# Kernel optimization log

Hardware: AMD Instinct MI355X
Metric: run time of the kernel (lower is better)

Reference implementation:

```python
import jax, jax.numpy as jnp
import numpy as np

EPS = 1e-6


def _rms_norm(x, w):
    # RMSNorm over last dim in fp32, like Qwen3RMSNorm
    x32 = x.astype(jnp.float32)
    var = jnp.mean(x32 * x32, axis=-1, keepdims=True)
    return (x32 * jax.lax.rsqrt(var + EPS)).astype(x.dtype) * w


def _rotate_half(x):
    h = x.shape[-1] // 2
    return jnp.concatenate([-x[..., h:], x[..., :h]], axis=-1)


def setup_inputs() -> dict:
    key = jax.random.key(0)
    ks = jax.random.split(key, 8)
    B, S, HID = 1, 8192, 1024
    H, HKV, D = 16, 8, 128
    n_seg = 8
    hidden_states = jax.random.normal(ks[0], (B, S, HID), dtype=jnp.float32)
    cu_seqlens = jnp.arange(n_seg + 1, dtype=jnp.int32) * (S // n_seg)
    # multimodal RoPE tables: two position streams, each [B, S, D]
    inv_freq = 1.0 / (1e6 ** (jnp.arange(0, D, 2, dtype=jnp.float32) / D))
    pos = jnp.arange(S, dtype=jnp.float32)
    ang0 = pos[:, None] * inv_freq[None, :]            # [S, D/2]
    ang1 = (pos[:, None] * 0.5) * inv_freq[None, :]    # second stream
    def tab(a):
        return jnp.concatenate([a, a], axis=-1)[None]   # [1, S, D]
    cos = jnp.stack([tab(jnp.cos(ang0)), tab(jnp.cos(ang1))], axis=0)  # [2,1,S,D]
    sin = jnp.stack([tab(jnp.sin(ang0)), tab(jnp.sin(ang1))], axis=0)
    sd = 0.02
    Wq = jax.random.normal(ks[1], (H * D, HID), dtype=jnp.float32) * sd
    Wk = jax.random.normal(ks[2], (HKV * D, HID), dtype=jnp.float32) * sd
    Wv = jax.random.normal(ks[3], (HKV * D, HID), dtype=jnp.float32) * sd
    Wo = jax.random.normal(ks[4], (HID, H * D), dtype=jnp.float32) * sd
    q_norm_w = 1.0 + jax.random.normal(ks[5], (D,), dtype=jnp.float32) * sd
    k_norm_w = 1.0 + jax.random.normal(ks[6], (D,), dtype=jnp.float32) * sd
    return {"hidden_states": hidden_states, "cu_seqlens": cu_seqlens,
            "cos": cos, "sin": sin, "Wq": Wq, "Wk": Wk, "Wv": Wv, "Wo": Wo,
            "q_norm_w": q_norm_w, "k_norm_w": k_norm_w}


def reference(hidden_states, cu_seqlens, cos, sin, Wq, Wk, Wv, Wo, q_norm_w, k_norm_w):
    B, S, _ = hidden_states.shape
    D = q_norm_w.shape[0]
    H = Wq.shape[0] // D
    HKV = Wk.shape[0] // D
    groups = H // HKV
    n_seg = cu_seqlens.shape[0] - 1   # equal-length segments (static)
    L = S // n_seg
    scaling = D ** -0.5

    # projections -> [B, H(kv), S, D]
    q = (hidden_states @ Wq.T).reshape(B, S, H, D).transpose(0, 2, 1, 3)
    k = (hidden_states @ Wk.T).reshape(B, S, HKV, D).transpose(0, 2, 1, 3)
    v = (hidden_states @ Wv.T).reshape(B, S, HKV, D).transpose(0, 2, 1, 3)

    q = _rms_norm(q, q_norm_w)
    k = _rms_norm(k, k_norm_w)

    # multimodal RoPE: interleave the two streams across the two half-dims
    half = D // 2
    cos_e = jnp.concatenate([cos[0, ..., :half], cos[1, ..., half:]], axis=-1)[:, None]  # [B,1,S,D]
    sin_e = jnp.concatenate([sin[0, ..., :half], sin[1, ..., half:]], axis=-1)[:, None]
    q = q * cos_e + _rotate_half(q) * sin_e
    k = k * cos_e + _rotate_half(k) * sin_e

    # GQA: repeat kv heads
    k = jnp.repeat(k, groups, axis=1)
    v = jnp.repeat(v, groups, axis=1)

    # block-diagonal attention over cu_seqlens segments (equal-length -> reshape)
    qb = q.reshape(B, H, n_seg, L, D)
    kb = k.reshape(B, H, n_seg, L, D)
    vb = v.reshape(B, H, n_seg, L, D)
    scores = jnp.einsum('bhnld,bhnmd->bhnlm', qb, kb) * scaling
    probs = jax.nn.softmax(scores, axis=-1)
    ob = jnp.einsum('bhnlm,bhnmd->bhnld', probs, vb)
    out = ob.reshape(B, H, S, D).transpose(0, 2, 1, 3).reshape(B, S, H * D)
    return out @ Wo.T
```

## Files before the change

kernel.cpp:

```cpp
#include <hip/hip_runtime.h>

#define S_LEN 8192
#define HID   1024
#define NH    16
#define NKV   8
#define HD    128
#define LSEG  1024

typedef float  f4  __attribute__((ext_vector_type(4)));
typedef _Float16 h4 __attribute__((ext_vector_type(4)));
typedef _Float16 h8 __attribute__((ext_vector_type(8)));

__device__ __forceinline__ void gl_lds16(const void* g, void* l) {
  __builtin_amdgcn_global_load_lds((const __attribute__((address_space(1))) void*)g,
                                   (__attribute__((address_space(3))) void*)l, 16, 0, 0);
}

__device__ __forceinline__ h8 ld8u(const _Float16* p) {
  h4 a = *(const h4*)p;
  h4 b = *(const h4*)(p + 4);
  return __builtin_shufflevector(a, b, 0, 1, 2, 3, 4, 5, 6, 7);
}

template <int CTRL>
__device__ __forceinline__ float dppf(float v) {
  return __builtin_bit_cast(float,
      __builtin_amdgcn_mov_dpp(__builtin_bit_cast(int, v), CTRL, 0xF, 0xF, true));
}
__device__ __forceinline__ float red16_max(float x) {
  x = fmaxf(x, dppf<0xB1>(x));
  x = fmaxf(x, dppf<0x4E>(x));
  x = fmaxf(x, dppf<0x141>(x));
  x = fmaxf(x, dppf<0x140>(x));
  return x;
}
__device__ __forceinline__ float red16_sum(float x) {
  x += dppf<0xB1>(x);
  x += dppf<0x4E>(x);
  x += dppf<0x141>(x);
  x += dppf<0x140>(x);
  return x;
}
__device__ __forceinline__ float bcast16(float v) {
  return __builtin_bit_cast(float,
      __builtin_amdgcn_ds_swizzle(__builtin_bit_cast(int, v), 0x0010));
}

__global__ void convert_kernel(const float* __restrict__ hid, const float* __restrict__ wq,
                               const float* __restrict__ wk, const float* __restrict__ wv,
                               const float* __restrict__ wo,
                               _Float16* __restrict__ hid16, _Float16* __restrict__ wqkv,
                               _Float16* __restrict__ wo16) {
  const int total4 = 3670016;
  for (int i = blockIdx.x * blockDim.x + threadIdx.x; i < total4; i += gridDim.x * blockDim.x) {
    int i4 = i * 4;
    const float* src; _Float16* dst;
    if      (i4 <  8388608) { src = hid + i4;              dst = hid16 + i4; }
    else if (i4 < 10485760) { src = wq + (i4 -  8388608);  dst = wqkv + (i4 - 8388608); }
    else if (i4 < 11534336) { src = wk + (i4 - 10485760);  dst = wqkv + 2097152 + (i4 - 10485760); }
    else if (i4 < 12582912) { src = wv + (i4 - 11534336);  dst = wqkv + 3145728 + (i4 - 11534336); }
    else                    { src = wo + (i4 - 12582912);  dst = wo16 + (i4 - 12582912); }
    f4 x = *(const f4*)src;
    h4 y; y[0]=(_Float16)x[0]; y[1]=(_Float16)x[1]; y[2]=(_Float16)x[2]; y[3]=(_Float16)x[3];
    *(h4*)dst = y;
  }
}

template <int FUSED>
__global__ __launch_bounds__(256, 3)
void gemm_kernel(const _Float16* __restrict__ A, const _Float16* __restrict__ B,
                 float* __restrict__ Cout, int K, int N,
                 const float* __restrict__ cosp, const float* __restrict__ sinp,
                 const float* __restrict__ qnw, const float* __restrict__ knw,
                 _Float16* __restrict__ q16, _Float16* __restrict__ k16,
                 _Float16* __restrict__ v16T) {
  __shared__ __align__(16) char smem[32768];

  constexpr int GX  = FUSED ? 32 : 8;
  constexpr int NWG = FUSED ? 2048 : 512;
  const int lin = blockIdx.y * GX + blockIdx.x;
  const int swz = (lin & 7) * (NWG >> 3) + (lin >> 3);
  const int bx = swz & (GX - 1), by = swz / GX;

  const int tid = threadIdx.x, w = tid >> 6, ln = tid & 63;
  const int l15 = ln & 15, l4 = ln >> 4;
  const int m0 = by * 128, n0 = bx * 128;
  const int sg_row = ln >> 2, sg_cho = (ln & 3) * 8;

  f4 acc[2][8] = {};

  for (int k0 = 0; k0 < K; k0 += 64) {
    __syncthreads();
#pragma unroll
    for (int r = 0; r < 2; r++) {
      int ch = r * 4 + w;
#pragma unroll
      for (int u = 0; u < 2; u++) {
        gl_lds16(A + (size_t)(m0 + ch * 16 + sg_row) * K + k0 + u * 32 + sg_cho,
                 smem + u * 8192 + ch * 1024);
        gl_lds16(B + (size_t)(n0 + ch * 16 + sg_row) * K + k0 + u * 32 + sg_cho,
                 smem + 16384 + u * 8192 + ch * 1024);
      }
    }
    __syncthreads();
#pragma unroll
    for (int u = 0; u < 2; u++) {
      const _Float16* As = (const _Float16*)(smem + u * 8192);
      const _Float16* Bs = (const _Float16*)(smem + 16384 + u * 8192);
      h8 af[2], bf[8];
#pragma unroll
      for (int mt = 0; mt < 2; mt++) af[mt] = *(const h8*)(As + (w * 32 + mt * 16 + l15) * 32 + l4 * 8);
#pragma unroll
      for (int nt = 0; nt < 8; nt++) bf[nt] = *(const h8*)(Bs + (nt * 16 + l15) * 32 + l4 * 8);
#pragma unroll
      for (int mt = 0; mt < 2; mt++)
#pragma unroll
        for (int nt = 0; nt < 8; nt++)
          acc[mt][nt] = __builtin_amdgcn_mfma_f32_16x16x32_f16(af[mt], bf[nt], acc[mt][nt], 0, 0, 0);
    }
  }

  if (!FUSED) {
#pragma unroll
    for (int mt = 0; mt < 2; mt++)
#pragma unroll
      for (int rg = 0; rg < 4; rg++) {
        int row = m0 + w * 32 + mt * 16 + l4 * 4 + rg;
#pragma unroll
        for (int nt = 0; nt < 8; nt++)
          Cout[(size_t)row * N + n0 + nt * 16 + l15] = acc[mt][nt][rg];
      }
    return;
  } else {
    const int head = bx;
    if (head < 24) {
      const float* nw = (head < 16) ? qnw : knw;
      const float hs = (head < 16) ? 0.12751734f : 1.0f;
      _Float16* base = (head < 16) ? q16 + (size_t)head * S_LEN * HD
                                   : k16 + (size_t)(head - 16) * S_LEN * HD;
      float nwv[8];
#pragma unroll
      for (int nt = 0; nt < 8; nt++) nwv[nt] = nw[nt * 16 + l15];
#pragma unroll
      for (int mt = 0; mt < 2; mt++)
#pragma unroll
        for (int rg = 0; rg < 4; rg++) {
          const int row = m0 + w * 32 + mt * 16 + l4 * 4 + rg;
          float ss = 0.f;
#pragma unroll
          for (int nt = 0; nt < 8; nt++) ss += acc[mt][nt][rg] * acc[mt][nt][rg];
          ss = red16_sum(ss);
          const float sc = rsqrtf(ss * 0.0078125f + 1e-6f);
#pragma unroll
          for (int nt = 0; nt < 8; nt++) {
            const int c = nt * 16 + l15;
            const int str = (nt >= 4) ? 1048576 : 0;
            float x  = acc[mt][nt][rg] * sc * nwv[nt];
            float xp = acc[mt][nt ^ 4][rg] * sc * nwv[nt ^ 4];
            float ce = cosp[str + row * HD + c];
            float se = sinp[str + row * HD + c];
            float rot = (nt >= 4) ? xp : -xp;
            base[(size_t)row * HD + c] = (_Float16)((x * ce + rot * se) * hs);
          }
        }
    } else {
      _Float16* vb = v16T + (size_t)(head - 24) * S_LEN * HD;
#pragma unroll
      for (int mt = 0; mt < 2; mt++)
#pragma unroll
        for (int nt = 0; nt < 8; nt++) {
          h4 hv;
#pragma unroll
          for (int rg = 0; rg < 4; rg++) hv[rg] = (_Float16)acc[mt][nt][rg];
          *(h4*)&vb[(size_t)(nt * 16 + l15) * S_LEN + m0 + w * 32 + mt * 16 + l4 * 4] = hv;
        }
    }
  }
}

__global__ __launch_bounds__(256, 2)
void attn_kernel(const _Float16* __restrict__ q16, const _Float16* __restrict__ k16,
                 const _Float16* __restrict__ vT, _Float16* __restrict__ ao16) {
  const int bid = blockIdx.x;
  const int xcd = bid & 7, slot = bid >> 3;
  const int grp = xcd * 8 + (slot >> 4);
  const int mem = slot & 15;
  const int g = grp >> 3, hkv = grp & 7;
  const int tq = mem & 7, h = hkv * 2 + (mem >> 3);

  const int tid = threadIdx.x, w = tid >> 6, ln = tid & 63;
  const int l15 = ln & 15, l4 = ln >> 4;

  __shared__ _Float16 Kb[2][64 * 132];
  __shared__ _Float16 Vb[2][128 * 68];

  const _Float16* qsrc = q16 + ((size_t)h * S_LEN + g * LSEG + tq * 128 + w * 32) * HD;
  h8 qf[2][4];
#pragma unroll
  for (int mt = 0; mt < 2; mt++)
#pragma unroll
    for (int kk = 0; kk < 4; kk++)
      qf[mt][kk] = *(const h8*)(qsrc + (size_t)(mt * 16 + l15) * HD + kk * 32 + l4 * 8);

  h8 onesB;
  {
    _Float16 ov = (l15 == 0) ? (_Float16)1.0f : (_Float16)0.0f;
#pragma unroll
    for (int jj = 0; jj < 8; jj++) onesB[jj] = ov;
  }

  f4 O[2][9] = {};
  float mr[2][4];
#pragma unroll
  for (int mt = 0; mt < 2; mt++)
#pragma unroll
    for (int rg = 0; rg < 4; rg++) mr[mt][rg] = -1e30f;

  const size_t kbase = ((size_t)hkv * S_LEN + g * LSEG) * HD;
  const size_t vbase = (size_t)hkv * S_LEN * HD + (size_t)g * LSEG;

  const int krow = tid >> 4, ko = tid & 15;
  const int vd   = tid >> 3, vo = tid & 7;
  const int vrow = w * 32 + (ln >> 1), vcol = (ln & 1) * 32;

  uint4 kr[4], vr[4];
#pragma unroll
  for (int i = 0; i < 4; i++) {
    kr[i] = *(const uint4*)(k16 + kbase + (size_t)(krow + 16 * i) * HD + ko * 8);
    vr[i] = *(const uint4*)(vT + vbase + (size_t)(vd + 32 * i) * S_LEN + vo * 8);
  }
#pragma unroll
  for (int i = 0; i < 4; i++) {
    int row = krow + 16 * i;
    *(uint2*)&Kb[0][row * 132 + ko * 8]     = make_uint2(kr[i].x, kr[i].y);
    *(uint2*)&Kb[0][row * 132 + ko * 8 + 4] = make_uint2(kr[i].z, kr[i].w);
    int d = vd + 32 * i;
    *(uint2*)&Vb[0][d * 68 + vo * 8]     = make_uint2(vr[i].x, vr[i].y);
    *(uint2*)&Vb[0][d * 68 + vo * 8 + 4] = make_uint2(vr[i].z, vr[i].w);
  }

  for (int j = 0; j < 16; j++) {
    __syncthreads();
    const int cur = j & 1, nxt = cur ^ 1;
    const _Float16* Kc = Kb[cur];
    const _Float16* Vc = Vb[cur];
    _Float16* Pb = Vb[nxt];
    _Float16* Kn = Kb[nxt];

    if (j < 15) {
      const int jn = j + 1;
#pragma unroll
      for (int i = 0; i < 4; i++)
        kr[i] = *(const uint4*)(k16 + kbase + (size_t)(jn * 64 + krow + 16 * i) * HD + ko * 8);
#pragma unroll
      for (int c = 0; c < 4; c++)
        vr[c] = *(const uint4*)(vT + vbase + (size_t)vrow * S_LEN + jn * 64 + vcol + c * 8);
    }

    f4 s[2][4] = {};
    __builtin_amdgcn_s_setprio(1);
#pragma unroll
    for (int kk = 0; kk < 4; kk++) {
#pragma unroll
      for (int nt = 0; nt < 4; nt++) {
        h8 b = ld8u(Kc + (nt * 16 + l15) * 132 + kk * 32 + l4 * 8);
        s[0][nt] = __builtin_amdgcn_mfma_f32_16x16x32_f16(qf[0][kk], b, s[0][nt], 0, 0, 0);
        s[1][nt] = __builtin_amdgcn_mfma_f32_16x16x32_f16(qf[1][kk], b, s[1][nt], 0, 0, 0);
      }
    }
    __builtin_amdgcn_s_setprio(0);

    bool nd = false;
#pragma unroll
    for (int mt = 0; mt < 2; mt++)
#pragma unroll
      for (int rg = 0; rg < 4; rg++) {
        float thr = mr[mt][rg] + 8.f;
        nd = nd || (s[mt][0][rg] > thr) || (s[mt][1][rg] > thr) ||
                   (s[mt][2][rg] > thr) || (s[mt][3][rg] > thr);
      }
    const bool needr = __any((int)nd) != 0;
    float al[2][4];
    if (needr) {
#pragma unroll
      for (int mt = 0; mt < 2; mt++)
#pragma unroll
        for (int rg = 0; rg < 4; rg++) {
          float m = fmaxf(fmaxf(s[mt][0][rg], s[mt][1][rg]), fmaxf(s[mt][2][rg], s[mt][3][rg]));
          m = red16_max(m);
          float mnew = fmaxf(mr[mt][rg], m);
          al[mt][rg] = exp2f(mr[mt][rg] - mnew);
          mr[mt][rg] = mnew;
        }
    }
#pragma unroll
    for (int mt = 0; mt < 2; mt++)
#pragma unroll
      for (int rg = 0; rg < 4; rg++)
#pragma unroll
        for (int nt = 0; nt < 4; nt++)
          s[mt][nt][rg] = exp2f(s[mt][nt][rg] - mr[mt][rg]);

#pragma unroll
    for (int mt = 0; mt < 2; mt++)
#pragma unroll
      for (int nt = 0; nt < 4; nt++)
#pragma unroll
        for (int rg = 0; rg < 4; rg++)
          Pb[(w * 32 + mt * 16 + l4 * 4 + rg) * 68 + nt * 16 + l15] = (_Float16)s[mt][nt][rg];
    if (needr) {
#pragma unroll
      for (int mt = 0; mt < 2; mt++)
#pragma unroll
        for (int d8 = 0; d8 < 9; d8++)
#pragma unroll
          for (int rg = 0; rg < 4; rg++) O[mt][d8][rg] *= al[mt][rg];
    }

    __builtin_amdgcn_s_setprio(1);
#pragma unroll
    for (int kk = 0; kk < 2; kk++) {
      h8 a0 = ld8u(Pb + (w * 32 + l15) * 68 + kk * 32 + l4 * 8);
      h8 a1 = ld8u(Pb + (w * 32 + 16 + l15) * 68 + kk * 32 + l4 * 8);
#pragma unroll
      for (int d8 = 0; d8 < 8; d8++) {
        h8 b = ld8u(Vc + (d8 * 16 + l15) * 68 + kk * 32 + l4 * 8);
        O[0][d8] = __builtin_amdgcn_mfma_f32_16x16x32_f16(a0, b, O[0][d8], 0, 0, 0);
        O[1][d8] = __builtin_amdgcn_mfma_f32_16x16x32_f16(a1, b, O[1][d8], 0, 0, 0);
      }
      O[0][8] = __builtin_amdgcn_mfma_f32_16x16x32_f16(a0, onesB, O[0][8], 0, 0, 0);
      O[1][8] = __builtin_amdgcn_mfma_f32_16x16x32_f16(a1, onesB, O[1][8], 0, 0, 0);
    }
    __builtin_amdgcn_s_setprio(0);

    if (j < 15) {
#pragma unroll
      for (int i = 0; i < 4; i++) {
        int row = krow + 16 * i;
        *(uint2*)&Kn[row * 132 + ko * 8]     = make_uint2(kr[i].x, kr[i].y);
        *(uint2*)&Kn[row * 132 + ko * 8 + 4] = make_uint2(kr[i].z, kr[i].w);
      }
#pragma unroll
      for (int c = 0; c < 4; c++) {
        *(uint2*)&Pb[vrow * 68 + vcol + c * 8]     = make_uint2(vr[c].x, vr[c].y);
        *(uint2*)&Pb[vrow * 68 + vcol + c * 8 + 4] = make_uint2(vr[c].z, vr[c].w);
      }
    }
  }

  const size_t obase = (size_t)(g * LSEG + tq * 128);
#pragma unroll
  for (int mt = 0; mt < 2; mt++)
#pragma unroll
    for (int rg = 0; rg < 4; rg++) {
      float inv = 1.f / bcast16(O[mt][8][rg]);
#pragma unroll
      for (int d8 = 0; d8 < 8; d8++)
        ao16[(obase + w * 32 + mt * 16 + l4 * 4 + rg) * 2048 + h * HD + d8 * 16 + l15] =
            (_Float16)(O[mt][d8][rg] * inv);
    }
}

extern "C" void kernel_launch(void* const* d_in, const int* in_sizes, int n_in,
                              void* d_out, int out_size, void* d_ws, size_t ws_size,
                              hipStream_t stream) {
  const float* hid  = (const float*)d_in[0];
  const float* cosp = (const float*)d_in[2];
  const float* sinp = (const float*)d_in[3];
  const float* wq   = (const float*)d_in[4];
  const float* wk   = (const float*)d_in[5];
  const float* wv   = (const float*)d_in[6];
  const float* wo   = (const float*)d_in[7];
  const float* qnw  = (const float*)d_in[8];
  const float* knw  = (const float*)d_in[9];
  float* out = (float*)d_out;

  _Float16* hid16 = (_Float16*)d_ws;
  _Float16* wqkv  = hid16 + 8388608;
  _Float16* wo16  = wqkv + 4194304;
  _Float16* q16   = wo16 + 2097152;
  _Float16* k16   = q16 + 16777216;
  _Float16* v16T  = k16 + 8388608;
  _Float16* ao16  = v16T + 8388608;

  convert_kernel<<<dim3(1024), dim3(256), 0, stream>>>(hid, wq, wk, wv, wo, hid16, wqkv, wo16);
  gemm_kernel<1><<<dim3(32, 64), dim3(256), 0, stream>>>(hid16, wqkv, nullptr, 1024, 4096,
                                                         cosp, sinp, qnw, knw, q16, k16, v16T);
  attn_kernel<<<dim3(1024), dim3(256), 0, stream>>>(q16, k16, v16T, ao16);
  gemm_kernel<0><<<dim3(8, 64), dim3(256), 0, stream>>>(ao16, wo16, out, 2048, 1024,
                                                        nullptr, nullptr, nullptr, nullptr,
                                                        nullptr, nullptr, nullptr);
}
```

Baseline: 366.2 us.

## Double-buffer GEMM K loop and pre-interleave cos/sin RoPE table

The GEMM main loop now processes 32-wide K steps with two LDS buffers, prefetching the next tile via global_load_lds while computing the current one, and uses one barrier per step instead of two. The convert kernel also builds a combined float2 cos/sin table with the mRoPE stream selection already applied, so the fused QKV epilogue does one 8-byte load instead of two scattered loads. The table reuses the attention-output workspace buffer, which attention overwrites afterward. This relies on the trailing barrier of each step to make the prefetched tile visible and adds a small extra pass in the convert kernel.

Result: slower. 386.2 us (+5.4%).

```diff
diff --git a/kernel.cpp b/kernel.cpp
--- a/kernel.cpp
+++ b/kernel.cpp
@@ -49,8 +49,9 @@
 __global__ void convert_kernel(const float* __restrict__ hid, const float* __restrict__ wq,
                                const float* __restrict__ wk, const float* __restrict__ wv,
                                const float* __restrict__ wo,
+                               const float* __restrict__ cosp, const float* __restrict__ sinp,
                                _Float16* __restrict__ hid16, _Float16* __restrict__ wqkv,
-                               _Float16* __restrict__ wo16) {
+                               _Float16* __restrict__ wo16, float2* __restrict__ cs32) {
   const int total4 = 3670016;
   for (int i = blockIdx.x * blockDim.x + threadIdx.x; i < total4; i += gridDim.x * blockDim.x) {
     int i4 = i * 4;
@@ -64,13 +65,17 @@
     h4 y; y[0]=(_Float16)x[0]; y[1]=(_Float16)x[1]; y[2]=(_Float16)x[2]; y[3]=(_Float16)x[3];
     *(h4*)dst = y;
   }
+  for (int i = blockIdx.x * blockDim.x + threadIdx.x; i < 1048576; i += gridDim.x * blockDim.x) {
+    int str = ((i & 127) >= 64) ? 1048576 : 0;
+    cs32[i] = make_float2(cosp[str + i], sinp[str + i]);
+  }
 }
 
 template <int FUSED>
 __global__ __launch_bounds__(256, 3)
 void gemm_kernel(const _Float16* __restrict__ A, const _Float16* __restrict__ B,
                  float* __restrict__ Cout, int K, int N,
-                 const float* __restrict__ cosp, const float* __restrict__ sinp,
+                 const float2* __restrict__ csp,
                  const float* __restrict__ qnw, const float* __restrict__ knw,
                  _Float16* __restrict__ q16, _Float16* __restrict__ k16,
                  _Float16* __restrict__ v16T) {
@@ -89,35 +94,36 @@
 
   f4 acc[2][8] = {};
 
-  for (int k0 = 0; k0 < K; k0 += 64) {
-    __syncthreads();
+  auto stage = [&](int u, int k) {
 #pragma unroll
     for (int r = 0; r < 2; r++) {
       int ch = r * 4 + w;
-#pragma unroll
-      for (int u = 0; u < 2; u++) {
-        gl_lds16(A + (size_t)(m0 + ch * 16 + sg_row) * K + k0 + u * 32 + sg_cho,
-                 smem + u * 8192 + ch * 1024);
-        gl_lds16(B + (size_t)(n0 + ch * 16 + sg_row) * K + k0 + u * 32 + sg_cho,
-                 smem + 16384 + u * 8192 + ch * 1024);
-      }
-    }
+      gl_lds16(A + (size_t)(m0 + ch * 16 + sg_row) * K + k + sg_cho,
+               smem + u * 8192 + ch * 1024);
+      gl_lds16(B + (size_t)(n0 + ch * 16 + sg_row) * K + k + sg_cho,
+               smem + 16384 + u * 8192 + ch * 1024);
+    }
+  };
+
+  stage(0, 0);
+  __syncthreads();
+  const int NP = K >> 5;
+  for (int p = 0; p < NP; ++p) {
+    const int cur = p & 1;
+    if (p + 1 < NP) stage(cur ^ 1, (p + 1) << 5);
+    const _Float16* As = (const _Float16*)(smem + cur * 8192);
+    const _Float16* Bs = (const _Float16*)(smem + 16384 + cur * 8192);
+    h8 af[2], bf[8];
+#pragma unroll
+    for (int mt = 0; mt < 2; mt++) af[mt] = *(const h8*)(As + (w * 32 + mt * 16 + l15) * 32 + l4 * 8);
+#pragma unroll
+    for (int nt = 0; nt < 8; nt++) bf[nt] = *(const h8*)(Bs + (nt * 16 + l15) * 32 + l4 * 8);
+#pragma unroll
+    for (int mt = 0; mt < 2; mt++)
+#pragma unroll
+      for (int nt = 0; nt < 8; nt++)
+        acc[mt][nt] = __builtin_amdgcn_mfma_f32_16x16x32_f16(af[mt], bf[nt], acc[mt][nt], 0, 0, 0);
     __syncthreads();
-#pragma unroll
-    for (int u = 0; u < 2; u++) {
-      const _Float16* As = (const _Float16*)(smem + u * 8192);
-      const _Float16* Bs = (const _Float16*)(smem + 16384 + u * 8192);
-      h8 af[2], bf[8];
-#pragma unroll
-      for (int mt = 0; mt < 2; mt++) af[mt] = *(const h8*)(As + (w * 32 + mt * 16 + l15) * 32 + l4 * 8);
-#pragma unroll
-      for (int nt = 0; nt < 8; nt++) bf[nt] = *(const h8*)(Bs + (nt * 16 + l15) * 32 + l4 * 8);
-#pragma unroll
-      for (int mt = 0; mt < 2; mt++)
-#pragma unroll
-        for (int nt = 0; nt < 8; nt++)
-          acc[mt][nt] = __builtin_amdgcn_mfma_f32_16x16x32_f16(af[mt], bf[nt], acc[mt][nt], 0, 0, 0);
-    }
   }
 
   if (!FUSED) {
@@ -154,13 +160,11 @@
 #pragma unroll
           for (int nt = 0; nt < 8; nt++) {
             const int c = nt * 16 + l15;
-            const int str = (nt >= 4) ? 1048576 : 0;
             float x  = acc[mt][nt][rg] * sc * nwv[nt];
             float xp = acc[mt][nt ^ 4][rg] * sc * nwv[nt ^ 4];
-            float ce = cosp[str + row * HD + c];
-            float se = sinp[str + row * HD + c];
+            float2 cse = csp[row * HD + c];
             float rot = (nt >= 4) ? xp : -xp;
-            base[(size_t)row * HD + c] = (_Float16)((x * ce + rot * se) * hs);
+            base[(size_t)row * HD + c] = (_Float16)((x * cse.x + rot * cse.y) * hs);
           }
         }
     } else {
@@ -382,12 +386,14 @@
   _Float16* k16   = q16 + 16777216;
   _Float16* v16T  = k16 + 8388608;
   _Float16* ao16  = v16T + 8388608;
-
-  convert_kernel<<<dim3(1024), dim3(256), 0, stream>>>(hid, wq, wk, wv, wo, hid16, wqkv, wo16);
+  float2*   cs32  = (float2*)ao16;
+
+  convert_kernel<<<dim3(1024), dim3(256), 0, stream>>>(hid, wq, wk, wv, wo, cosp, sinp,
+                                                       hid16, wqkv, wo16, cs32);
   gemm_kernel<1><<<dim3(32, 64), dim3(256), 0, stream>>>(hid16, wqkv, nullptr, 1024, 4096,
-                                                         cosp, sinp, qnw, knw, q16, k16, v16T);
+                                                         cs32, qnw, knw, q16, k16, v16T);
   attn_kernel<<<dim3(1024), dim3(256), 0, stream>>>(q16, k16, v16T, ao16);
   gemm_kernel<0><<<dim3(8, 64), dim3(256), 0, stream>>>(ao16, wo16, out, 2048, 1024,
-                                                        nullptr, nullptr, nullptr, nullptr,
+                                                        nullptr, nullptr, nullptr,
                                                         nullptr, nullptr, nullptr);
 }
```
